# Kernel optimization log

Hardware: AMD Instinct MI355X
Metric: run time of the kernel (lower is better)

The kernel has to match this reference:

```python
import jax, jax.numpy as jnp
import numpy as np

N = 50000        # nodes
E = 800000       # edges
D_IN = 128       # input feature dim
HID = 64         # hidden_dim
HEADS = 4
OUT = 2          # output_dim (fraud / not-fraud)
BN_EPS = 1e-5
NEG_SLOPE = 0.2  # PyG GATv2Conv default


def setup_inputs() -> dict:
    key = jax.random.key(0)
    ks = jax.random.split(key, 16)
    g = lambda k, shape, s=0.05: (jax.random.normal(k, shape, jnp.float32) * s)
    HC = HEADS * HID  # 256
    return {
        "x": jax.random.normal(ks[0], (N, D_IN), jnp.float32),
        "edge_index": jax.random.randint(ks[1], (2, E), 0, N),
        # input projection
        "W_in": g(ks[2], (D_IN, HID)), "b_in": jnp.zeros((HID,), jnp.float32),
        # GATv2 layer 0: HID -> HID, 4 heads (concat -> 256)
        "Wl0": g(ks[3], (HID, HC)), "Wr0": g(ks[4], (HID, HC)),
        "att0": g(ks[5], (HEADS, HID)), "bias0": jnp.zeros((HC,), jnp.float32),
        # GATv2 layer 1: 256 -> HID, 4 heads (concat -> 256)
        "Wl1": g(ks[6], (HC, HC)), "Wr1": g(ks[7], (HC, HC)),
        "att1": g(ks[8], (HEADS, HID)), "bias1": jnp.zeros((HC,), jnp.float32),
        # GATv2 layer 2: 256 -> OUT, 1 head
        "Wl2": g(ks[9], (HC, OUT)), "Wr2": g(ks[10], (HC, OUT)),
        "att2": g(ks[11], (1, OUT)), "bias2": jnp.zeros((OUT,), jnp.float32),
        # BatchNorm (eval mode: running stats) for the first num_layers-1 = 2 layers
        "bn_gamma": jnp.ones((2, HC), jnp.float32),
        "bn_beta": jnp.zeros((2, HC), jnp.float32),
        "bn_mean": jnp.zeros((2, HC), jnp.float32),
        "bn_var": jnp.ones((2, HC), jnp.float32),
    }


def _gatv2(h, src, dst, Wl, Wr, att, bias):
    """PyG GATv2Conv (concat=True, negative_slope=0.2). src->dst messages."""
    n = h.shape[0]
    heads, c = att.shape
    xl = (h @ Wl).reshape(n, heads, c)   # source transform
    xr = (h @ Wr).reshape(n, heads, c)   # target transform
    e = jax.nn.leaky_relu(xl[src] + xr[dst], NEG_SLOPE)       # [E, H, C]
    logits = jnp.einsum('ehc,hc->eh', e, att)                 # [E, H]
    # segment softmax over incoming edges of each destination node
    m = jax.ops.segment_max(logits, dst, num_segments=n)      # [N, H]
    ex = jnp.exp(logits - m[dst])
    denom = jax.ops.segment_sum(ex, dst, num_segments=n)
    alpha = ex / denom[dst]                                   # [E, H]
    out = jax.ops.segment_sum(xl[src] * alpha[..., None], dst, num_segments=n)
    return out.reshape(n, heads * c) + bias


def _bn_eval(h, gamma, beta, mean, var):
    return gamma * (h - mean) * jax.lax.rsqrt(var + BN_EPS) + beta


def reference(x, edge_index, W_in, b_in, Wl0, Wr0, att0, bias0,
              Wl1, Wr1, att1, bias1, Wl2, Wr2, att2, bias2,
              bn_gamma, bn_beta, bn_mean, bn_var):
    n = x.shape[0]
    loop = jnp.arange(n)
    src = jnp.concatenate([edge_index[0], loop])  # PyG add_self_loops=True
    dst = jnp.concatenate([edge_index[1], loop])

    h = jax.nn.relu(x @ W_in + b_in)              # dropout is identity in eval

    # layer 0 (no residual: 64 != 256)
    h = _gatv2(h, src, dst, Wl0, Wr0, att0, bias0)
    h = jax.nn.relu(_bn_eval(h, bn_gamma[0], bn_beta[0], bn_mean[0], bn_var[0]))

    # layer 1 (residual: 256 == 256)
    h_prev = h
    h = _gatv2(h, src, dst, Wl1, Wr1, att1, bias1)
    h = jax.nn.relu(_bn_eval(h, bn_gamma[1], bn_beta[1], bn_mean[1], bn_var[1]))
    h = h + h_prev

    # output layer, 1 head
    h = _gatv2(h, src, dst, Wl2, Wr2, att2, bias2)
    return jax.nn.log_softmax(h, axis=1)
```

## Files before the change

### kernel.cpp

```cpp
#include <hip/hip_runtime.h>
#include <hip/hip_bf16.h>
#include <math.h>


using h16     = _Float16;
using half2v  = __attribute__((ext_vector_type(2))) h16;
using half4v  = __attribute__((ext_vector_type(4))) h16;
using half8   = __attribute__((ext_vector_type(8))) h16;
using floatx2 = __attribute__((ext_vector_type(2))) float;
using floatx4 = __attribute__((ext_vector_type(4))) float;

__device__ __forceinline__ float lrelu(float x) { return x > 0.f ? x : 0.2f * x; }

__device__ __forceinline__ half2v shfl_xor_h2(half2v v, int mask) {
    float f = __builtin_bit_cast(float, v);
    f = __shfl_xor(f, mask, 64);
    return __builtin_bit_cast(half2v, f);
}

__global__ void hist_dst(const int* __restrict__ ei, int E, int* __restrict__ deg) {
    int e = blockIdx.x * blockDim.x + threadIdx.x;
    if (e < E) atomicAdd(&deg[ei[E + e]], 1);
}

__global__ __launch_bounds__(256) void scan_blk(const int* __restrict__ deg,
                                                int* __restrict__ rowstart,
                                                int* __restrict__ bsum, int N) {
    int t = blockIdx.x * 256 + threadIdx.x;
    int lane = threadIdx.x & 63, wid = threadIdx.x >> 6;
    int v = (t < N) ? ((deg[t] + 4) & ~3) : 0;
    int x = v;
#pragma unroll
    for (int off = 1; off < 64; off <<= 1) {
        int y = __shfl_up(x, off, 64);
        if (lane >= off) x += y;
    }
    __shared__ int wsum[4];
    if (lane == 63) wsum[wid] = x;
    __syncthreads();
    int add = 0;
#pragma unroll
    for (int w = 0; w < 4; ++w) if (w < wid) add += wsum[w];
    int incl = x + add;
    if (t < N) rowstart[t] = incl - v;
    if (threadIdx.x == 255) bsum[blockIdx.x] = incl;
}

__global__ __launch_bounds__(256) void scan_off(int* __restrict__ bsum, int NB) {
    int t = threadIdx.x;
    int lane = t & 63, wid = t >> 6;
    int v = (t < NB) ? bsum[t] : 0;
    int x = v;
#pragma unroll
    for (int off = 1; off < 64; off <<= 1) {
        int y = __shfl_up(x, off, 64);
        if (lane >= off) x += y;
    }
    __shared__ int wsum[4];
    if (lane == 63) wsum[wid] = x;
    __syncthreads();
    int add = 0;
#pragma unroll
    for (int w = 0; w < 4; ++w) if (w < wid) add += wsum[w];
    if (t < NB) bsum[t] = x + add - v;
}

__global__ void add_off(const int* __restrict__ bsum, const int* __restrict__ deg,
                        int* __restrict__ rowstart, int* __restrict__ cursor,
                        int* __restrict__ csr_src, int N) {
    int t = blockIdx.x * 256 + threadIdx.x;
    if (t >= N) return;
    int r = rowstart[t] + bsum[blockIdx.x];
    rowstart[t] = r;
    cursor[t] = r;
    int dg = deg[t];
    int npad = (dg + 4) & ~3;
    for (int k = dg; k < npad; ++k) csr_src[r + k] = t;
}

__global__ void scatter_src(const int* __restrict__ ei, int E,
                            int* __restrict__ cursor, int* __restrict__ csr_src) {
    int e = blockIdx.x * blockDim.x + threadIdx.x;
    if (e >= E) return;
    int d = ei[E + e];
    int pos = atomicAdd(&cursor[d], 1);
    csr_src[pos] = ei[e];
}

__device__ __forceinline__ void pack_one(const float* __restrict__ W,
                                         h16* __restrict__ Wp,
                                         int t, int K, int NC) {
    int j = t & 7;
    int l = (t >> 3) & 63;
    int rest = t >> 9;
    int NT = NC >> 4;
    int nt = rest % NT;
    int kc = rest / NT;
    int row = kc * 32 + (l >> 4) * 8 + j;
    int col = nt * 16 + (l & 15);
    Wp[t] = (h16)W[(size_t)row * NC + col];
}

__global__ void pack_all(const float* __restrict__ W_in,
                         const float* __restrict__ Wl0, const float* __restrict__ Wr0,
                         const float* __restrict__ Wl1, const float* __restrict__ Wr1,
                         h16* __restrict__ P_in,
                         h16* __restrict__ P_l0, h16* __restrict__ P_r0,
                         h16* __restrict__ P_l1, h16* __restrict__ P_r1,
                         const float4* __restrict__ x, half4v* __restrict__ xh, int n4,
                         int* __restrict__ deg, int N) {
    int t = blockIdx.x * blockDim.x + threadIdx.x;
    if (t < 8192)        pack_one(W_in, P_in, t, 128, 64);
    else if (t < 24576)  pack_one(Wl0, P_l0, t - 8192, 64, 256);
    else if (t < 40960)  pack_one(Wr0, P_r0, t - 24576, 64, 256);
    else if (t < 106496) pack_one(Wl1, P_l1, t - 40960, 256, 256);
    else if (t < 172032) pack_one(Wr1, P_r1, t - 106496, 256, 256);
    else if (t < 172032 + n4) {
        int u = t - 172032;
        float4 v = x[u];
        half4v o = { (h16)v.x, (h16)v.y, (h16)v.z, (h16)v.w };
        xh[u] = o;
    } else {
        int u = t - 172032 - n4;
        if (u < N) deg[u] = 0;
    }
}

template<int KC, int NT, bool RELU, bool DUAL>
__global__ __launch_bounds__(256) void gemm_lds(
        const h16* __restrict__ Xh,
        const h16* __restrict__ Wp0, const h16* __restrict__ Wp1,
        const float* __restrict__ bias,
        h16* __restrict__ out0, h16* __restrict__ out1, int M) {
    constexpr int K = KC * 32;
    constexpr int ldo = NT * 16;
    constexpr int CHUNK8 = NT * 64;
    constexpr int PER_THR = CHUNK8 / 256;
    __shared__ half8 wbuf[2][CHUNK8];

    const h16* Wp = (DUAL && blockIdx.y) ? Wp1 : Wp0;
    h16* outp = (DUAL && blockIdx.y) ? out1 : out0;
    const half8* WG = (const half8*)Wp;

    const int tid = threadIdx.x;
    const int wid = tid >> 6, lane = tid & 63;
    const int quad = lane >> 4, li = lane & 15;
    const int r0 = blockIdx.x * 64 + wid * 16;
    int arow = r0 + li; if (arow >= M) arow = M - 1;
    const half8* A8 = (const half8*)Xh + (size_t)arow * (K / 8) + quad;

    floatx4 acc[NT];
#pragma unroll
    for (int t = 0; t < NT; ++t) acc[t] = (floatx4){0.f, 0.f, 0.f, 0.f};

    half8 st[PER_THR];
#pragma unroll
    for (int i = 0; i < PER_THR; ++i) st[i] = WG[i * 256 + tid];
#pragma unroll
    for (int i = 0; i < PER_THR; ++i) wbuf[0][i * 256 + tid] = st[i];
    __syncthreads();

#pragma unroll
    for (int kc = 0; kc < KC; ++kc) {
        int cur = kc & 1;
        if (kc + 1 < KC) {
#pragma unroll
            for (int i = 0; i < PER_THR; ++i)
                st[i] = WG[(size_t)(kc + 1) * CHUNK8 + i * 256 + tid];
        }
        half8 a = A8[kc * 4];
#pragma unroll
        for (int nt = 0; nt < NT; ++nt) {
            half8 b = wbuf[cur][nt * 64 + lane];
            acc[nt] = __builtin_amdgcn_mfma_f32_16x16x32_f16(a, b, acc[nt], 0, 0, 0);
        }
        if (kc + 1 < KC) {
#pragma unroll
            for (int i = 0; i < PER_THR; ++i) wbuf[cur ^ 1][i * 256 + tid] = st[i];
        }
        __syncthreads();
    }

#pragma unroll
    for (int nt = 0; nt < NT; ++nt) {
#pragma unroll
        for (int reg = 0; reg < 4; ++reg) {
            int rr = r0 + quad * 4 + reg;
            if (rr >= M) continue;
            float v = acc[nt][reg];
            if (RELU) v = fmaxf(v + bias[nt * 16 + li], 0.f);
            outp[(size_t)rr * ldo + nt * 16 + li] = (h16)v;
        }
    }
}

__global__ void attn4_bn(int N, const h16* __restrict__ XL,
                         const h16* __restrict__ XR,
                         const float* __restrict__ att,
                         const int* __restrict__ rowstart, const int* __restrict__ deg,
                         const int* __restrict__ csr_src,
                         const float* __restrict__ gamma, const float* __restrict__ beta,
                         const float* __restrict__ mean, const float* __restrict__ var,
                         const float* __restrict__ bias, const h16* __restrict__ resid,
                         h16* __restrict__ outb) {
    int wv = blockIdx.x * (blockDim.x >> 6) + (threadIdx.x >> 6);
    int d0 = wv * 2;
    if (d0 >= N) return;
    int lane = threadIdx.x & 63;
    int sl   = lane & 31;
    int dh   = d0 + (lane >> 5);
    bool dvalid = dh < N;
    int dr = dvalid ? dh : d0;

    int start = rowstart[dr];
    int dg    = deg[dr];
    int nreal = dg + 1;
    int npad  = (dg + 4) & ~3;
    int npmax = max(npad, __shfl_xor(npad, 32, 64));

    union H8 { uint4 u; half2v h[4]; };
    H8 bv, wt;
    bv.u = *(const uint4*)(XR + (size_t)dr * 256 + sl * 8);
    {
        const float* ar = att + (sl >> 3) * 64 + (sl & 7) * 8;
        float4 wa = *(const float4*)ar;
        float4 wb = *(const float4*)(ar + 4);
        wt.h[0] = half2v{(h16)wa.x, (h16)wa.y};
        wt.h[1] = half2v{(h16)wa.z, (h16)wa.w};
        wt.h[2] = half2v{(h16)wb.x, (h16)wb.y};
        wt.h[3] = half2v{(h16)wb.z, (h16)wb.w};
    }
    const h16 k02 = (h16)0.2f;
    const uint4* XLv = (const uint4*)XL;

    auto ep = [&](const H8& x) -> h16 {
        half2v q = half2v{(h16)0, (h16)0};
#pragma unroll
        for (int j = 0; j < 4; ++j) {
            half2v e  = x.h[j] + bv.h[j];
            half2v lr = __builtin_elementwise_max(e, e * k02);
            q += lr * wt.h[j];
        }
        return q.x + q.y;
    };

    float l = 0.f;
    half2v acc[4] = {half2v{(h16)0,(h16)0}, half2v{(h16)0,(h16)0},
                     half2v{(h16)0,(h16)0}, half2v{(h16)0,(h16)0}};

    int4 iv = *(const int4*)(csr_src + start);
    for (int i = 0; i < npmax; i += 4) {
        int4 cur = iv;
        if (i + 4 < npmax) {
            int nxt = min(i + 4, npad - 4);
            iv = *(const int4*)(csr_src + start + nxt);
        }
        H8 x0, x1, x2, x3;
        x0.u = XLv[(size_t)(unsigned)cur.x * 32 + sl];
        x1.u = XLv[(size_t)(unsigned)cur.y * 32 + sl];
        x2.u = XLv[(size_t)(unsigned)cur.z * 32 + sl];
        x3.u = XLv[(size_t)(unsigned)cur.w * 32 + sl];
        half2v p01 = { ep(x0), ep(x1) };
        half2v p23 = { ep(x2), ep(x3) };
#pragma unroll
        for (int s = 1; s < 8; s <<= 1) {
            p01 += shfl_xor_h2(p01, s);
            p23 += shfl_xor_h2(p23, s);
        }
        int rem = nreal - i;
        float e0 = (rem > 0) ? __expf((float)p01.x) : 0.f;
        float e1 = (rem > 1) ? __expf((float)p01.y) : 0.f;
        float e2 = (rem > 2) ? __expf((float)p23.x) : 0.f;
        float e3 = (rem > 3) ? __expf((float)p23.y) : 0.f;
        l += (e0 + e1) + (e2 + e3);
        h16 h0 = (h16)e0, h1 = (h16)e1, h2 = (h16)e2, h3 = (h16)e3;
        half2v eb0 = {h0,h0}, eb1 = {h1,h1}, eb2 = {h2,h2}, eb3 = {h3,h3};
#pragma unroll
        for (int j = 0; j < 4; ++j) {
            acc[j] += eb0 * x0.h[j];
            acc[j] += eb1 * x1.h[j];
            acc[j] += eb2 * x2.h[j];
            acc[j] += eb3 * x3.h[j];
        }
    }

    float inv = 1.f / l;
    float oc[8];
#pragma unroll
    for (int j = 0; j < 4; ++j) { oc[2*j] = (float)acc[j].x; oc[2*j+1] = (float)acc[j].y; }
    const float4* g4  = (const float4*)gamma;
    const float4* be4 = (const float4*)beta;
    const float4* mu4 = (const float4*)mean;
    const float4* va4 = (const float4*)var;
    const float4* bi4 = (const float4*)bias;
    float o[8];
#pragma unroll
    for (int q = 0; q < 2; ++q) {
        float4 g  = g4[sl*2+q],  bb = be4[sl*2+q], mu = mu4[sl*2+q];
        float4 va = va4[sl*2+q], bi = bi4[sl*2+q];
        float s0 = g.x * rsqrtf(va.x + 1e-5f);
        float s1 = g.y * rsqrtf(va.y + 1e-5f);
        float s2 = g.z * rsqrtf(va.z + 1e-5f);
        float s3 = g.w * rsqrtf(va.w + 1e-5f);
        o[q*4+0] = fmaxf(oc[q*4+0]*inv*s0 + (bi.x-mu.x)*s0 + bb.x, 0.f);
        o[q*4+1] = fmaxf(oc[q*4+1]*inv*s1 + (bi.y-mu.y)*s1 + bb.y, 0.f);
        o[q*4+2] = fmaxf(oc[q*4+2]*inv*s2 + (bi.z-mu.z)*s2 + bb.z, 0.f);
        o[q*4+3] = fmaxf(oc[q*4+3]*inv*s3 + (bi.w-mu.w)*s3 + bb.w, 0.f);
    }
    if (resid) {
        H8 rv; rv.u = *(const uint4*)(resid + (size_t)dr * 256 + sl * 8);
#pragma unroll
        for (int j = 0; j < 4; ++j) {
            o[2*j]   += (float)rv.h[j].x;
            o[2*j+1] += (float)rv.h[j].y;
        }
    }
    if (dvalid) {
        H8 ov;
#pragma unroll
        for (int j = 0; j < 4; ++j) ov.h[j] = half2v{(h16)o[2*j], (h16)o[2*j+1]};
        *(uint4*)(outb + (size_t)dh * 256 + sl * 8) = ov.u;
    }
}

__global__ void gemm2_wave(const h16* __restrict__ X, const float* __restrict__ Wl,
                           const float* __restrict__ Wr, float* __restrict__ xl2,
                           float* __restrict__ xr2, int N) {
    int t = blockIdx.x * blockDim.x + threadIdx.x;
    int n = t >> 4;
    int sl = t & 15;
    if (n >= N) return;
    const half4v* Xr = (const half4v*)(X + (size_t)n * 256);
    const float4* Wl4 = (const float4*)Wl;
    const float4* Wr4 = (const float4*)Wr;
    float l0 = 0.f, l1 = 0.f, r0 = 0.f, r1 = 0.f;
#pragma unroll
    for (int j = 0; j < 4; ++j) {
        int idx = sl + j * 16;
        half4v xh = Xr[idx];
        float4 xv = { (float)xh.x, (float)xh.y, (float)xh.z, (float)xh.w };
        float4 wa = Wl4[idx * 2];
        float4 wb = Wl4[idx * 2 + 1];
        l0 += xv.x * wa.x + xv.y * wa.z + xv.z * wb.x + xv.w * wb.z;
        l1 += xv.x * wa.y + xv.y * wa.w + xv.z * wb.y + xv.w * wb.w;
        wa = Wr4[idx * 2]; wb = Wr4[idx * 2 + 1];
        r0 += xv.x * wa.x + xv.y * wa.z + xv.z * wb.x + xv.w * wb.z;
        r1 += xv.x * wa.y + xv.y * wa.w + xv.z * wb.y + xv.w * wb.w;
    }
#pragma unroll
    for (int off = 1; off < 16; off <<= 1) {
        l0 += __shfl_xor(l0, off, 64);
        l1 += __shfl_xor(l1, off, 64);
        r0 += __shfl_xor(r0, off, 64);
        r1 += __shfl_xor(r1, off, 64);
    }
    if (sl == 0) {
        xl2[n * 2] = l0; xl2[n * 2 + 1] = l1;
        xr2[n * 2] = r0; xr2[n * 2 + 1] = r1;
    }
}

__global__ void attn1_16(int N, const float* __restrict__ xl2, const float* __restrict__ xr2,
                         const float* __restrict__ att, const float* __restrict__ bias,
                         const int* __restrict__ rowstart, const int* __restrict__ deg,
                         const int* __restrict__ csr_src, float* __restrict__ out) {
    int t = blockIdx.x * blockDim.x + threadIdx.x;
    int d = t >> 4, sl = t & 15;
    if (d >= N) return;
    float a0 = att[0], a1 = att[1];
    float2 xr = ((const float2*)xr2)[d];
    float b0 = xr.x, b1 = xr.y;
    int st = rowstart[d];
    int nreal = deg[d] + 1;
    int npad  = (deg[d] + 4) & ~3;
    float l = 0.f, ac0 = 0.f, ac1 = 0.f;
    for (int i = sl; i < npad; i += 16) {
        int s = csr_src[st + i];
        float2 xv = ((const float2*)xl2)[s];
        float q = lrelu(xv.x + b0) * a0 + lrelu(xv.y + b1) * a1;
        float e = (i < nreal) ? __expf(q) : 0.f;
        l += e; ac0 += e * xv.x; ac1 += e * xv.y;
    }
#pragma unroll
    for (int off = 1; off < 16; off <<= 1) {
        l   += __shfl_xor(l, off, 64);
        ac0 += __shfl_xor(ac0, off, 64);
        ac1 += __shfl_xor(ac1, off, 64);
    }
    if (sl == 0) {
        float inv = 1.f / l;
        float v0 = ac0 * inv + bias[0];
        float v1 = ac1 * inv + bias[1];
        float mx = fmaxf(v0, v1);
        float lse = mx + logf(__expf(v0 - mx) + __expf(v1 - mx));
        out[d * 2] = v0 - lse;
        out[d * 2 + 1] = v1 - lse;
    }
}

extern "C" void kernel_launch(void* const* d_in, const int* in_sizes, int n_in,
                              void* d_out, int out_size, void* d_ws, size_t ws_size,
                              hipStream_t stream) {
    const float* x        = (const float*)d_in[0];
    const int*   ei       = (const int*)  d_in[1];
    const float* W_in     = (const float*)d_in[2];
    const float* b_in     = (const float*)d_in[3];
    const float* Wl0      = (const float*)d_in[4];
    const float* Wr0      = (const float*)d_in[5];
    const float* att0     = (const float*)d_in[6];
    const float* bias0    = (const float*)d_in[7];
    const float* Wl1      = (const float*)d_in[8];
    const float* Wr1      = (const float*)d_in[9];
    const float* att1     = (const float*)d_in[10];
    const float* bias1    = (const float*)d_in[11];
    const float* Wl2      = (const float*)d_in[12];
    const float* Wr2      = (const float*)d_in[13];
    const float* att2     = (const float*)d_in[14];
    const float* bias2    = (const float*)d_in[15];
    const float* bn_gamma = (const float*)d_in[16];
    const float* bn_beta  = (const float*)d_in[17];
    const float* bn_mean  = (const float*)d_in[18];
    const float* bn_var   = (const float*)d_in[19];

    const int N  = in_sizes[0] / 128;
    const int E  = in_sizes[1] / 2;
    const int NB = (N + 255) / 256;

    float* ws = (float*)d_ws;
    size_t off = 0;
    float* XL2  = ws + off; off += (size_t)N * 2;
    float* XR2  = ws + off; off += (size_t)N * 2;
    h16* Ah   = (h16*)(ws + off); off += (size_t)N * 128;
    h16* Bh   = (h16*)(ws + off); off += (size_t)N * 128;
    h16* Ch   = (h16*)(ws + off); off += (size_t)N * 128;
    h16* Dh   = (h16*)(ws + off); off += (size_t)N * 128;
    h16* H0h  = (h16*)(ws + off); off += (size_t)N * 32;
    h16* xh   = (h16*)(ws + off); off += (size_t)N * 64;
    h16* Wp_in = (h16*)(ws + off); off += 4096;
    h16* Wp_l0 = (h16*)(ws + off); off += 8192;
    h16* Wp_r0 = (h16*)(ws + off); off += 8192;
    h16* Wp_l1 = (h16*)(ws + off); off += 32768;
    h16* Wp_r1 = (h16*)(ws + off); off += 32768;
    int* ip = (int*)(ws + off);
    int* deg      = ip;              ip += N;
    int* rowstart = ip;              ip += N;
    int* cursor   = ip;              ip += N;
    int* bsum     = ip;              ip += NB;
    int* csr_src  = ip;              ip += E + 4 * N + 64;

    const int PACK_T = 172032 + N * 32 + N;
    pack_all<<<(PACK_T + 255) / 256, 256, 0, stream>>>(
        W_in, Wl0, Wr0, Wl1, Wr1, Wp_in, Wp_l0, Wp_r0, Wp_l1, Wp_r1,
        (const float4*)x, (half4v*)xh, N * 32, deg, N);

    hist_dst<<<(E + 255) / 256, 256, 0, stream>>>(ei, E, deg);
    scan_blk<<<NB, 256, 0, stream>>>(deg, rowstart, bsum, N);
    scan_off<<<1, 256, 0, stream>>>(bsum, NB);
    add_off<<<NB, 256, 0, stream>>>(bsum, deg, rowstart, cursor, csr_src, N);
    scatter_src<<<(E + 255) / 256, 256, 0, stream>>>(ei, E, cursor, csr_src);

    const int GBM = (N + 63) / 64;

    gemm_lds<4, 4, true, false><<<GBM, 256, 0, stream>>>(
        xh, Wp_in, nullptr, b_in, H0h, nullptr, N);

    gemm_lds<2, 16, false, true><<<dim3(GBM, 2), 256, 0, stream>>>(
        H0h, Wp_l0, Wp_r0, nullptr, Ah, Bh, N);
    attn4_bn<<<(N + 7) / 8, 256, 0, stream>>>(N, Ah, Bh, att0, rowstart, deg, csr_src,
                                              bn_gamma, bn_beta, bn_mean, bn_var,
                                              bias0, nullptr, Ch);

    gemm_lds<8, 16, false, true><<<dim3(GBM, 2), 256, 0, stream>>>(
        Ch, Wp_l1, Wp_r1, nullptr, Ah, Bh, N);
    attn4_bn<<<(N + 7) / 8, 256, 0, stream>>>(N, Ah, Bh, att1, rowstart, deg, csr_src,
                                              bn_gamma + 256, bn_beta + 256, bn_mean + 256,
                                              bn_var + 256, bias1, Ch, Dh);

    gemm2_wave<<<(N * 16 + 255) / 256, 256, 0, stream>>>(Dh, Wl2, Wr2, XL2, XR2, N);
    attn1_16<<<(N * 16 + 255) / 256, 256, 0, stream>>>(N, XL2, XR2, att2, bias2,
                                                       rowstart, deg, csr_src, (float*)d_out);
}
```

Baseline: 405.4 us.

## Degree-bin node permutation, 4 nodes per wave, fuse hist and scatter into other kernels

Nodes are bucketed by padded in-degree into 32 bins, and the resulting permutation drives attn4_bn so each wave handles 4 similar-degree destinations with 16 lanes per node, instead of 2 arbitrary nodes with 32 lanes each. The degree histogram is folded into pack_all and the edge scatter into a combined kernel with the input GEMM, with a memset replacing the in-kernel deg clearing. The aim is to cut load imbalance across a wave and reduce launch count. In exchange, each lane does more per-lane work and uses more registers, and the permuted output writes are scattered.

Result: slower. 982.6 us (+142.4%).

```diff
diff --git a/kernel.cpp b/kernel.cpp
--- a/kernel.cpp
+++ b/kernel.cpp
@@ -18,17 +18,17 @@
     return __builtin_bit_cast(half2v, f);
 }
 
-__global__ void hist_dst(const int* __restrict__ ei, int E, int* __restrict__ deg) {
-    int e = blockIdx.x * blockDim.x + threadIdx.x;
-    if (e < E) atomicAdd(&deg[ei[E + e]], 1);
-}
-
 __global__ __launch_bounds__(256) void scan_blk(const int* __restrict__ deg,
                                                 int* __restrict__ rowstart,
-                                                int* __restrict__ bsum, int N) {
+                                                int* __restrict__ bsum,
+                                                int* __restrict__ bins, int N) {
     int t = blockIdx.x * 256 + threadIdx.x;
     int lane = threadIdx.x & 63, wid = threadIdx.x >> 6;
-    int v = (t < N) ? ((deg[t] + 4) & ~3) : 0;
+    int v = 0;
+    if (t < N) {
+        v = (deg[t] + 4) & ~3;
+        atomicAdd(&bins[min(v >> 2, 31)], 1);
+    }
     int x = v;
 #pragma unroll
     for (int off = 1; off < 64; off <<= 1) {
@@ -46,7 +46,9 @@
     if (threadIdx.x == 255) bsum[blockIdx.x] = incl;
 }
 
-__global__ __launch_bounds__(256) void scan_off(int* __restrict__ bsum, int NB) {
+__global__ __launch_bounds__(256) void scan_off(int* __restrict__ bsum, int NB,
+                                                const int* __restrict__ bins,
+                                                int* __restrict__ bincur) {
     int t = threadIdx.x;
     int lane = t & 63, wid = t >> 6;
     int v = (t < NB) ? bsum[t] : 0;
@@ -63,11 +65,22 @@
 #pragma unroll
     for (int w = 0; w < 4; ++w) if (w < wid) add += wsum[w];
     if (t < NB) bsum[t] = x + add - v;
+    if (t < 32) {
+        int b = bins[t];
+        int xb = b;
+#pragma unroll
+        for (int off2 = 1; off2 < 32; off2 <<= 1) {
+            int y = __shfl_up(xb, off2, 64);
+            if (t >= off2) xb += y;
+        }
+        bincur[t] = xb - b;
+    }
 }
 
 __global__ void add_off(const int* __restrict__ bsum, const int* __restrict__ deg,
                         int* __restrict__ rowstart, int* __restrict__ cursor,
-                        int* __restrict__ csr_src, int N) {
+                        int* __restrict__ csr_src,
+                        int* __restrict__ bincur, int* __restrict__ perm, int N) {
     int t = blockIdx.x * 256 + threadIdx.x;
     if (t >= N) return;
     int r = rowstart[t] + bsum[blockIdx.x];
@@ -76,15 +89,8 @@
     int dg = deg[t];
     int npad = (dg + 4) & ~3;
     for (int k = dg; k < npad; ++k) csr_src[r + k] = t;
-}
-
-__global__ void scatter_src(const int* __restrict__ ei, int E,
-                            int* __restrict__ cursor, int* __restrict__ csr_src) {
-    int e = blockIdx.x * blockDim.x + threadIdx.x;
-    if (e >= E) return;
-    int d = ei[E + e];
-    int pos = atomicAdd(&cursor[d], 1);
-    csr_src[pos] = ei[e];
+    int pos = atomicAdd(&bincur[min(npad >> 2, 31)], 1);
+    perm[pos] = t;
 }
 
 __device__ __forceinline__ void pack_one(const float* __restrict__ W,
@@ -108,7 +114,7 @@
                          h16* __restrict__ P_l0, h16* __restrict__ P_r0,
                          h16* __restrict__ P_l1, h16* __restrict__ P_r1,
                          const float4* __restrict__ x, half4v* __restrict__ xh, int n4,
-                         int* __restrict__ deg, int N) {
+                         const int* __restrict__ ei, int E, int* __restrict__ deg) {
     int t = blockIdx.x * blockDim.x + threadIdx.x;
     if (t < 8192)        pack_one(W_in, P_in, t, 128, 64);
     else if (t < 24576)  pack_one(Wl0, P_l0, t - 8192, 64, 256);
@@ -122,7 +128,71 @@
         xh[u] = o;
     } else {
         int u = t - 172032 - n4;
-        if (u < N) deg[u] = 0;
+        if (u < E) atomicAdd(&deg[ei[E + u]], 1);
+    }
+}
+
+template<int KC, int NT, bool RELU>
+__device__ __forceinline__ void gemm_body(const h16* __restrict__ Xh,
+                                          const h16* __restrict__ Wp,
+                                          const float* __restrict__ bias,
+                                          h16* __restrict__ outp, int M, int bx) {
+    constexpr int K = KC * 32;
+    constexpr int ldo = NT * 16;
+    constexpr int CHUNK8 = NT * 64;
+    constexpr int PER_THR = CHUNK8 / 256;
+    __shared__ half8 wbuf[2][CHUNK8];
+
+    const half8* WG = (const half8*)Wp;
+    const int tid = threadIdx.x;
+    const int wid = tid >> 6, lane = tid & 63;
+    const int quad = lane >> 4, li = lane & 15;
+    const int r0 = bx * 64 + wid * 16;
+    int arow = r0 + li; if (arow >= M) arow = M - 1;
+    const half8* A8 = (const half8*)Xh + (size_t)arow * (K / 8) + quad;
+
+    floatx4 acc[NT];
+#pragma unroll
+    for (int t = 0; t < NT; ++t) acc[t] = (floatx4){0.f, 0.f, 0.f, 0.f};
+
+    half8 st[PER_THR];
+#pragma unroll
+    for (int i = 0; i < PER_THR; ++i) st[i] = WG[i * 256 + tid];
+#pragma unroll
+    for (int i = 0; i < PER_THR; ++i) wbuf[0][i * 256 + tid] = st[i];
+    __syncthreads();
+
+#pragma unroll
+    for (int kc = 0; kc < KC; ++kc) {
+        int cur = kc & 1;
+        if (kc + 1 < KC) {
+#pragma unroll
+            for (int i = 0; i < PER_THR; ++i)
+                st[i] = WG[(size_t)(kc + 1) * CHUNK8 + i * 256 + tid];
+        }
+        half8 a = A8[kc * 4];
+#pragma unroll
+        for (int nt = 0; nt < NT; ++nt) {
+            half8 b = wbuf[cur][nt * 64 + lane];
+            acc[nt] = __builtin_amdgcn_mfma_f32_16x16x32_f16(a, b, acc[nt], 0, 0, 0);
+        }
+        if (kc + 1 < KC) {
+#pragma unroll
+            for (int i = 0; i < PER_THR; ++i) wbuf[cur ^ 1][i * 256 + tid] = st[i];
+        }
+        __syncthreads();
+    }
+
+#pragma unroll
+    for (int nt = 0; nt < NT; ++nt) {
+#pragma unroll
+        for (int reg = 0; reg < 4; ++reg) {
+            int rr = r0 + quad * 4 + reg;
+            if (rr >= M) continue;
+            float v = acc[nt][reg];
+            if (RELU) v = fmaxf(v + bias[nt * 16 + li], 0.f);
+            outp[(size_t)rr * ldo + nt * 16 + li] = (h16)v;
+        }
     }
 }
 
@@ -132,71 +202,32 @@
         const h16* __restrict__ Wp0, const h16* __restrict__ Wp1,
         const float* __restrict__ bias,
         h16* __restrict__ out0, h16* __restrict__ out1, int M) {
-    constexpr int K = KC * 32;
-    constexpr int ldo = NT * 16;
-    constexpr int CHUNK8 = NT * 64;
-    constexpr int PER_THR = CHUNK8 / 256;
-    __shared__ half8 wbuf[2][CHUNK8];
-
     const h16* Wp = (DUAL && blockIdx.y) ? Wp1 : Wp0;
     h16* outp = (DUAL && blockIdx.y) ? out1 : out0;
-    const half8* WG = (const half8*)Wp;
-
-    const int tid = threadIdx.x;
-    const int wid = tid >> 6, lane = tid & 63;
-    const int quad = lane >> 4, li = lane & 15;
-    const int r0 = blockIdx.x * 64 + wid * 16;
-    int arow = r0 + li; if (arow >= M) arow = M - 1;
-    const half8* A8 = (const half8*)Xh + (size_t)arow * (K / 8) + quad;
-
-    floatx4 acc[NT];
-#pragma unroll
-    for (int t = 0; t < NT; ++t) acc[t] = (floatx4){0.f, 0.f, 0.f, 0.f};
-
-    half8 st[PER_THR];
-#pragma unroll
-    for (int i = 0; i < PER_THR; ++i) st[i] = WG[i * 256 + tid];
-#pragma unroll
-    for (int i = 0; i < PER_THR; ++i) wbuf[0][i * 256 + tid] = st[i];
-    __syncthreads();
-
-#pragma unroll
-    for (int kc = 0; kc < KC; ++kc) {
-        int cur = kc & 1;
-        if (kc + 1 < KC) {
-#pragma unroll
-            for (int i = 0; i < PER_THR; ++i)
-                st[i] = WG[(size_t)(kc + 1) * CHUNK8 + i * 256 + tid];
-        }
-        half8 a = A8[kc * 4];
-#pragma unroll
-        for (int nt = 0; nt < NT; ++nt) {
-            half8 b = wbuf[cur][nt * 64 + lane];
-            acc[nt] = __builtin_amdgcn_mfma_f32_16x16x32_f16(a, b, acc[nt], 0, 0, 0);
-        }
-        if (kc + 1 < KC) {
-#pragma unroll
-            for (int i = 0; i < PER_THR; ++i) wbuf[cur ^ 1][i * 256 + tid] = st[i];
-        }
-        __syncthreads();
-    }
-
-#pragma unroll
-    for (int nt = 0; nt < NT; ++nt) {
-#pragma unroll
-        for (int reg = 0; reg < 4; ++reg) {
-            int rr = r0 + quad * 4 + reg;
-            if (rr >= M) continue;
-            float v = acc[nt][reg];
-            if (RELU) v = fmaxf(v + bias[nt * 16 + li], 0.f);
-            outp[(size_t)rr * ldo + nt * 16 + li] = (h16)v;
-        }
+    gemm_body<KC, NT, RELU>(Xh, Wp, bias, outp, M, blockIdx.x);
+}
+
+__global__ __launch_bounds__(256) void scatter_gemm0(
+        const int* __restrict__ ei, int E,
+        int* __restrict__ cursor, int* __restrict__ csr_src, int GS,
+        const h16* __restrict__ xh, const h16* __restrict__ Wp_in,
+        const float* __restrict__ b_in, h16* __restrict__ H0h, int M) {
+    if ((int)blockIdx.x < GS) {
+        int e = blockIdx.x * 256 + threadIdx.x;
+        if (e < E) {
+            int d = ei[E + e];
+            int pos = atomicAdd(&cursor[d], 1);
+            csr_src[pos] = ei[e];
+        }
+    } else {
+        gemm_body<4, 4, true>(xh, Wp_in, b_in, H0h, M, blockIdx.x - GS);
     }
 }
 
 __global__ void attn4_bn(int N, const h16* __restrict__ XL,
                          const h16* __restrict__ XR,
                          const float* __restrict__ att,
+                         const int* __restrict__ perm,
                          const int* __restrict__ rowstart, const int* __restrict__ deg,
                          const int* __restrict__ csr_src,
                          const float* __restrict__ gamma, const float* __restrict__ beta,
@@ -204,39 +235,40 @@
                          const float* __restrict__ bias, const h16* __restrict__ resid,
                          h16* __restrict__ outb) {
     int wv = blockIdx.x * (blockDim.x >> 6) + (threadIdx.x >> 6);
-    int d0 = wv * 2;
-    if (d0 >= N) return;
+    if (wv * 4 >= N) return;
     int lane = threadIdx.x & 63;
-    int sl   = lane & 31;
-    int dh   = d0 + (lane >> 5);
-    bool dvalid = dh < N;
-    int dr = dvalid ? dh : d0;
-
-    int start = rowstart[dr];
-    int dg    = deg[dr];
+    int sl   = lane & 15;
+    int idx  = wv * 4 + (lane >> 4);
+    bool dvalid = idx < N;
+    int dh = perm[dvalid ? idx : (N - 1)];
+
+    int start = rowstart[dh];
+    int dg    = deg[dh];
     int nreal = dg + 1;
     int npad  = (dg + 4) & ~3;
-    int npmax = max(npad, __shfl_xor(npad, 32, 64));
-
-    union H8 { uint4 u; half2v h[4]; };
-    H8 bv, wt;
-    bv.u = *(const uint4*)(XR + (size_t)dr * 256 + sl * 8);
+    int m1    = max(npad, __shfl_xor(npad, 16, 64));
+    int npmax = max(m1, __shfl_xor(m1, 32, 64));
+
+    union H16 { uint4 u[2]; half2v h[8]; };
+    H16 bv, wt;
+    bv.u[0] = *(const uint4*)(XR + (size_t)dh * 256 + sl * 16);
+    bv.u[1] = *(const uint4*)(XR + (size_t)dh * 256 + sl * 16 + 8);
     {
-        const float* ar = att + (sl >> 3) * 64 + (sl & 7) * 8;
-        float4 wa = *(const float4*)ar;
-        float4 wb = *(const float4*)(ar + 4);
-        wt.h[0] = half2v{(h16)wa.x, (h16)wa.y};
-        wt.h[1] = half2v{(h16)wa.z, (h16)wa.w};
-        wt.h[2] = half2v{(h16)wb.x, (h16)wb.y};
-        wt.h[3] = half2v{(h16)wb.z, (h16)wb.w};
+        const float* ar = att + sl * 16;
+#pragma unroll
+        for (int q = 0; q < 4; ++q) {
+            float4 w = *(const float4*)(ar + q * 4);
+            wt.h[2*q]   = half2v{(h16)w.x, (h16)w.y};
+            wt.h[2*q+1] = half2v{(h16)w.z, (h16)w.w};
+        }
     }
     const h16 k02 = (h16)0.2f;
     const uint4* XLv = (const uint4*)XL;
 
-    auto ep = [&](const H8& x) -> h16 {
-        half2v q = half2v{(h16)0, (h16)0};
-#pragma unroll
-        for (int j = 0; j < 4; ++j) {
+    auto ep = [&](const H16& x) -> h16 {
+        half2v q{(h16)0, (h16)0};
+#pragma unroll
+        for (int j = 0; j < 8; ++j) {
             half2v e  = x.h[j] + bv.h[j];
             half2v lr = __builtin_elementwise_max(e, e * k02);
             q += lr * wt.h[j];
@@ -245,8 +277,9 @@
     };
 
     float l = 0.f;
-    half2v acc[4] = {half2v{(h16)0,(h16)0}, half2v{(h16)0,(h16)0},
-                     half2v{(h16)0,(h16)0}, half2v{(h16)0,(h16)0}};
+    half2v acc[8];
+#pragma unroll
+    for (int j = 0; j < 8; ++j) acc[j] = half2v{(h16)0, (h16)0};
 
     int4 iv = *(const int4*)(csr_src + start);
     for (int i = 0; i < npmax; i += 4) {
@@ -255,15 +288,19 @@
             int nxt = min(i + 4, npad - 4);
             iv = *(const int4*)(csr_src + start + nxt);
         }
-        H8 x0, x1, x2, x3;
-        x0.u = XLv[(size_t)(unsigned)cur.x * 32 + sl];
-        x1.u = XLv[(size_t)(unsigned)cur.y * 32 + sl];
-        x2.u = XLv[(size_t)(unsigned)cur.z * 32 + sl];
-        x3.u = XLv[(size_t)(unsigned)cur.w * 32 + sl];
+        H16 x0, x1, x2, x3;
+        size_t a0 = (size_t)(unsigned)cur.x * 32 + sl * 2;
+        size_t a1 = (size_t)(unsigned)cur.y * 32 + sl * 2;
+        size_t a2 = (size_t)(unsigned)cur.z * 32 + sl * 2;
+        size_t a3 = (size_t)(unsigned)cur.w * 32 + sl * 2;
+        x0.u[0] = XLv[a0]; x0.u[1] = XLv[a0 + 1];
+        x1.u[0] = XLv[a1]; x1.u[1] = XLv[a1 + 1];
+        x2.u[0] = XLv[a2]; x2.u[1] = XLv[a2 + 1];
+        x3.u[0] = XLv[a3]; x3.u[1] = XLv[a3 + 1];
         half2v p01 = { ep(x0), ep(x1) };
         half2v p23 = { ep(x2), ep(x3) };
 #pragma unroll
-        for (int s = 1; s < 8; s <<= 1) {
+        for (int s = 1; s < 4; s <<= 1) {
             p01 += shfl_xor_h2(p01, s);
             p23 += shfl_xor_h2(p23, s);
         }
@@ -274,9 +311,9 @@
         float e3 = (rem > 3) ? __expf((float)p23.y) : 0.f;
         l += (e0 + e1) + (e2 + e3);
         h16 h0 = (h16)e0, h1 = (h16)e1, h2 = (h16)e2, h3 = (h16)e3;
-        half2v eb0 = {h0,h0}, eb1 = {h1,h1}, eb2 = {h2,h2}, eb3 = {h3,h3};
-#pragma unroll
-        for (int j = 0; j < 4; ++j) {
+        half2v eb0{h0,h0}, eb1{h1,h1}, eb2{h2,h2}, eb3{h3,h3};
+#pragma unroll
+        for (int j = 0; j < 8; ++j) {
             acc[j] += eb0 * x0.h[j];
             acc[j] += eb1 * x1.h[j];
             acc[j] += eb2 * x2.h[j];
@@ -285,19 +322,20 @@
     }
 
     float inv = 1.f / l;
-    float oc[8];
-#pragma unroll
-    for (int j = 0; j < 4; ++j) { oc[2*j] = (float)acc[j].x; oc[2*j+1] = (float)acc[j].y; }
+    float oc[16];
+#pragma unroll
+    for (int j = 0; j < 8; ++j) { oc[2*j] = (float)acc[j].x; oc[2*j+1] = (float)acc[j].y; }
     const float4* g4  = (const float4*)gamma;
     const float4* be4 = (const float4*)beta;
     const float4* mu4 = (const float4*)mean;
     const float4* va4 = (const float4*)var;
     const float4* bi4 = (const float4*)bias;
-    float o[8];
-#pragma unroll
-    for (int q = 0; q < 2; ++q) {
-        float4 g  = g4[sl*2+q],  bb = be4[sl*2+q], mu = mu4[sl*2+q];
-        float4 va = va4[sl*2+q], bi = bi4[sl*2+q];
+    float o[16];
+#pragma unroll
+    for (int q = 0; q < 4; ++q) {
+        int ci = sl * 4 + q;
+        float4 g  = g4[ci], bb = be4[ci], mu = mu4[ci];
+        float4 va = va4[ci], bi = bi4[ci];
         float s0 = g.x * rsqrtf(va.x + 1e-5f);
         float s1 = g.y * rsqrtf(va.y + 1e-5f);
         float s2 = g.z * rsqrtf(va.z + 1e-5f);
@@ -308,18 +346,21 @@
         o[q*4+3] = fmaxf(oc[q*4+3]*inv*s3 + (bi.w-mu.w)*s3 + bb.w, 0.f);
     }
     if (resid) {
-        H8 rv; rv.u = *(const uint4*)(resid + (size_t)dr * 256 + sl * 8);
-#pragma unroll
-        for (int j = 0; j < 4; ++j) {
+        H16 rv;
+        rv.u[0] = *(const uint4*)(resid + (size_t)dh * 256 + sl * 16);
+        rv.u[1] = *(const uint4*)(resid + (size_t)dh * 256 + sl * 16 + 8);
+#pragma unroll
+        for (int j = 0; j < 8; ++j) {
             o[2*j]   += (float)rv.h[j].x;
             o[2*j+1] += (float)rv.h[j].y;
         }
     }
     if (dvalid) {
-        H8 ov;
-#pragma unroll
-        for (int j = 0; j < 4; ++j) ov.h[j] = half2v{(h16)o[2*j], (h16)o[2*j+1]};
-        *(uint4*)(outb + (size_t)dh * 256 + sl * 8) = ov.u;
+        H16 ov;
+#pragma unroll
+        for (int j = 0; j < 8; ++j) ov.h[j] = half2v{(h16)o[2*j], (h16)o[2*j+1]};
+        *(uint4*)(outb + (size_t)dh * 256 + sl * 16)     = ov.u[0];
+        *(uint4*)(outb + (size_t)dh * 256 + sl * 16 + 8) = ov.u[1];
     }
 }
 
@@ -443,38 +484,45 @@
     h16* Wp_r1 = (h16*)(ws + off); off += 32768;
     int* ip = (int*)(ws + off);
     int* deg      = ip;              ip += N;
+    int* bins     = ip;              ip += 32;
+    int* bincur   = ip;              ip += 32;
     int* rowstart = ip;              ip += N;
     int* cursor   = ip;              ip += N;
     int* bsum     = ip;              ip += NB;
+    int* perm     = ip;              ip += N;
     int* csr_src  = ip;              ip += E + 4 * N + 64;
 
-    const int PACK_T = 172032 + N * 32 + N;
+    hipMemsetAsync(deg, 0, (size_t)(N + 32) * sizeof(int), stream);
+
+    const int PACK_T = 172032 + N * 32 + E;
     pack_all<<<(PACK_T + 255) / 256, 256, 0, stream>>>(
         W_in, Wl0, Wr0, Wl1, Wr1, Wp_in, Wp_l0, Wp_r0, Wp_l1, Wp_r1,
-        (const float4*)x, (half4v*)xh, N * 32, deg, N);
-
-    hist_dst<<<(E + 255) / 256, 256, 0, stream>>>(ei, E, deg);
-    scan_blk<<<NB, 256, 0, stream>>>(deg, rowstart, bsum, N);
-    scan_off<<<1, 256, 0, stream>>>(bsum, NB);
-    add_off<<<NB, 256, 0, stream>>>(bsum, deg, rowstart, cursor, csr_src, N);
-    scatter_src<<<(E + 255) / 256, 256, 0, stream>>>(ei, E, cursor, csr_src);
+        (const float4*)x, (half4v*)xh, N * 32, ei, E, deg);
+
+    scan_blk<<<NB, 256, 0, stream>>>(deg, rowstart, bsum, bins, N);
+    scan_off<<<1, 256, 0, stream>>>(bsum, NB, bins, bincur);
+    add_off<<<NB, 256, 0, stream>>>(bsum, deg, rowstart, cursor, csr_src,
+                                    bincur, perm, N);
 
     const int GBM = (N + 63) / 64;
-
-    gemm_lds<4, 4, true, false><<<GBM, 256, 0, stream>>>(
-        xh, Wp_in, nullptr, b_in, H0h, nullptr, N);
+    const int GS  = (E + 255) / 256;
+
+    scatter_gemm0<<<GS + GBM, 256, 0, stream>>>(ei, E, cursor, csr_src, GS,
+                                                xh, Wp_in, b_in, H0h, N);
 
     gemm_lds<2, 16, false, true><<<dim3(GBM, 2), 256, 0, stream>>>(
         H0h, Wp_l0, Wp_r0, nullptr, Ah, Bh, N);
-    attn4_bn<<<(N + 7) / 8, 256, 0, stream>>>(N, Ah, Bh, att0, rowstart, deg, csr_src,
-                                              bn_gamma, bn_beta, bn_mean, bn_var,
-                                              bias0, nullptr, Ch);
+    attn4_bn<<<(N + 15) / 16, 256, 0, stream>>>(N, Ah, Bh, att0, perm,
+                                                rowstart, deg, csr_src,
+                                                bn_gamma, bn_beta, bn_mean, bn_var,
+                                                bias0, nullptr, Ch);
 
     gemm_lds<8, 16, false, true><<<dim3(GBM, 2), 256, 0, stream>>>(
         Ch, Wp_l1, Wp_r1, nullptr, Ah, Bh, N);
-    attn4_bn<<<(N + 7) / 8, 256, 0, stream>>>(N, Ah, Bh, att1, rowstart, deg, csr_src,
-                                              bn_gamma + 256, bn_beta + 256, bn_mean + 256,
-                                              bn_var + 256, bias1, Ch, Dh);
+    attn4_bn<<<(N + 15) / 16, 256, 0, stream>>>(N, Ah, Bh, att1, perm,
+                                                rowstart, deg, csr_src,
+                                                bn_gamma + 256, bn_beta + 256, bn_mean + 256,
+                                                bn_var + 256, bias1, Ch, Dh);
 
     gemm2_wave<<<(N * 16 + 255) / 256, 256, 0, stream>>>(Dh, Wl2, Wr2, XL2, XR2, N);
     attn1_16<<<(N * 16 + 255) / 256, 256, 0, stream>>>(N, XL2, XR2, att2, bias2,
```

## Fuse degree histogram into pack kernel and scatter into input GEMM

Applied to the files above, without the earlier changes.

Degree zeroing moves to a memset so the destination-degree histogram can run inside the weight/feature packing kernel. The CSR scatter kernel and the input projection GEMM are merged into one launch, with block ranges split between edge scattering (4 edges per thread, loads batched for memory-level parallelism) and GEMM tiles. This cuts two kernel launches and lets independent work overlap. The cost is mixed block roles, and the gemm body is refactored into a shared device function.

Result: faster. 397.1 us (-2.1%).

```diff
diff --git a/kernel.cpp b/kernel.cpp
--- a/kernel.cpp
+++ b/kernel.cpp
@@ -16,11 +16,6 @@
     float f = __builtin_bit_cast(float, v);
     f = __shfl_xor(f, mask, 64);
     return __builtin_bit_cast(half2v, f);
-}
-
-__global__ void hist_dst(const int* __restrict__ ei, int E, int* __restrict__ deg) {
-    int e = blockIdx.x * blockDim.x + threadIdx.x;
-    if (e < E) atomicAdd(&deg[ei[E + e]], 1);
 }
 
 __global__ __launch_bounds__(256) void scan_blk(const int* __restrict__ deg,
@@ -76,15 +71,6 @@
     int dg = deg[t];
     int npad = (dg + 4) & ~3;
     for (int k = dg; k < npad; ++k) csr_src[r + k] = t;
-}
-
-__global__ void scatter_src(const int* __restrict__ ei, int E,
-                            int* __restrict__ cursor, int* __restrict__ csr_src) {
-    int e = blockIdx.x * blockDim.x + threadIdx.x;
-    if (e >= E) return;
-    int d = ei[E + e];
-    int pos = atomicAdd(&cursor[d], 1);
-    csr_src[pos] = ei[e];
 }
 
 __device__ __forceinline__ void pack_one(const float* __restrict__ W,
@@ -108,7 +94,7 @@
                          h16* __restrict__ P_l0, h16* __restrict__ P_r0,
                          h16* __restrict__ P_l1, h16* __restrict__ P_r1,
                          const float4* __restrict__ x, half4v* __restrict__ xh, int n4,
-                         int* __restrict__ deg, int N) {
+                         const int* __restrict__ ei, int E, int* __restrict__ deg) {
     int t = blockIdx.x * blockDim.x + threadIdx.x;
     if (t < 8192)        pack_one(W_in, P_in, t, 128, 64);
     else if (t < 24576)  pack_one(Wl0, P_l0, t - 8192, 64, 256);
@@ -122,7 +108,71 @@
         xh[u] = o;
     } else {
         int u = t - 172032 - n4;
-        if (u < N) deg[u] = 0;
+        if (u < E) atomicAdd(&deg[ei[E + u]], 1);
+    }
+}
+
+template<int KC, int NT, bool RELU>
+__device__ __forceinline__ void gemm_body(const h16* __restrict__ Xh,
+                                          const h16* __restrict__ Wp,
+                                          const float* __restrict__ bias,
+                                          h16* __restrict__ outp, int M, int bx) {
+    constexpr int K = KC * 32;
+    constexpr int ldo = NT * 16;
+    constexpr int CHUNK8 = NT * 64;
+    constexpr int PER_THR = CHUNK8 / 256;
+    __shared__ half8 wbuf[2][CHUNK8];
+
+    const half8* WG = (const half8*)Wp;
+    const int tid = threadIdx.x;
+    const int wid = tid >> 6, lane = tid & 63;
+    const int quad = lane >> 4, li = lane & 15;
+    const int r0 = bx * 64 + wid * 16;
+    int arow = r0 + li; if (arow >= M) arow = M - 1;
+    const half8* A8 = (const half8*)Xh + (size_t)arow * (K / 8) + quad;
+
+    floatx4 acc[NT];
+#pragma unroll
+    for (int t = 0; t < NT; ++t) acc[t] = (floatx4){0.f, 0.f, 0.f, 0.f};
+
+    half8 st[PER_THR];
+#pragma unroll
+    for (int i = 0; i < PER_THR; ++i) st[i] = WG[i * 256 + tid];
+#pragma unroll
+    for (int i = 0; i < PER_THR; ++i) wbuf[0][i * 256 + tid] = st[i];
+    __syncthreads();
+
+#pragma unroll
+    for (int kc = 0; kc < KC; ++kc) {
+        int cur = kc & 1;
+        if (kc + 1 < KC) {
+#pragma unroll
+            for (int i = 0; i < PER_THR; ++i)
+                st[i] = WG[(size_t)(kc + 1) * CHUNK8 + i * 256 + tid];
+        }
+        half8 a = A8[kc * 4];
+#pragma unroll
+        for (int nt = 0; nt < NT; ++nt) {
+            half8 b = wbuf[cur][nt * 64 + lane];
+            acc[nt] = __builtin_amdgcn_mfma_f32_16x16x32_f16(a, b, acc[nt], 0, 0, 0);
+        }
+        if (kc + 1 < KC) {
+#pragma unroll
+            for (int i = 0; i < PER_THR; ++i) wbuf[cur ^ 1][i * 256 + tid] = st[i];
+        }
+        __syncthreads();
+    }
+
+#pragma unroll
+    for (int nt = 0; nt < NT; ++nt) {
+#pragma unroll
+        for (int reg = 0; reg < 4; ++reg) {
+            int rr = r0 + quad * 4 + reg;
+            if (rr >= M) continue;
+            float v = acc[nt][reg];
+            if (RELU) v = fmaxf(v + bias[nt * 16 + li], 0.f);
+            outp[(size_t)rr * ldo + nt * 16 + li] = (h16)v;
+        }
     }
 }
 
@@ -132,65 +182,37 @@
         const h16* __restrict__ Wp0, const h16* __restrict__ Wp1,
         const float* __restrict__ bias,
         h16* __restrict__ out0, h16* __restrict__ out1, int M) {
-    constexpr int K = KC * 32;
-    constexpr int ldo = NT * 16;
-    constexpr int CHUNK8 = NT * 64;
-    constexpr int PER_THR = CHUNK8 / 256;
-    __shared__ half8 wbuf[2][CHUNK8];
-
     const h16* Wp = (DUAL && blockIdx.y) ? Wp1 : Wp0;
     h16* outp = (DUAL && blockIdx.y) ? out1 : out0;
-    const half8* WG = (const half8*)Wp;
-
-    const int tid = threadIdx.x;
-    const int wid = tid >> 6, lane = tid & 63;
-    const int quad = lane >> 4, li = lane & 15;
-    const int r0 = blockIdx.x * 64 + wid * 16;
-    int arow = r0 + li; if (arow >= M) arow = M - 1;
-    const half8* A8 = (const half8*)Xh + (size_t)arow * (K / 8) + quad;
-
-    floatx4 acc[NT];
-#pragma unroll
-    for (int t = 0; t < NT; ++t) acc[t] = (floatx4){0.f, 0.f, 0.f, 0.f};
-
-    half8 st[PER_THR];
-#pragma unroll
-    for (int i = 0; i < PER_THR; ++i) st[i] = WG[i * 256 + tid];
-#pragma unroll
-    for (int i = 0; i < PER_THR; ++i) wbuf[0][i * 256 + tid] = st[i];
-    __syncthreads();
-
-#pragma unroll
-    for (int kc = 0; kc < KC; ++kc) {
-        int cur = kc & 1;
-        if (kc + 1 < KC) {
-#pragma unroll
-            for (int i = 0; i < PER_THR; ++i)
-                st[i] = WG[(size_t)(kc + 1) * CHUNK8 + i * 256 + tid];
-        }
-        half8 a = A8[kc * 4];
-#pragma unroll
-        for (int nt = 0; nt < NT; ++nt) {
-            half8 b = wbuf[cur][nt * 64 + lane];
-            acc[nt] = __builtin_amdgcn_mfma_f32_16x16x32_f16(a, b, acc[nt], 0, 0, 0);
-        }
-        if (kc + 1 < KC) {
-#pragma unroll
-            for (int i = 0; i < PER_THR; ++i) wbuf[cur ^ 1][i * 256 + tid] = st[i];
-        }
-        __syncthreads();
-    }
-
-#pragma unroll
-    for (int nt = 0; nt < NT; ++nt) {
-#pragma unroll
-        for (int reg = 0; reg < 4; ++reg) {
-            int rr = r0 + quad * 4 + reg;
-            if (rr >= M) continue;
-            float v = acc[nt][reg];
-            if (RELU) v = fmaxf(v + bias[nt * 16 + li], 0.f);
-            outp[(size_t)rr * ldo + nt * 16 + li] = (h16)v;
-        }
+    gemm_body<KC, NT, RELU>(Xh, Wp, bias, outp, M, blockIdx.x);
+}
+
+__global__ __launch_bounds__(256) void scatter_gemm0(
+        const int* __restrict__ ei, int E,
+        int* __restrict__ cursor, int* __restrict__ csr_src, int GS,
+        const h16* __restrict__ xh, const h16* __restrict__ Wp_in,
+        const float* __restrict__ b_in, h16* __restrict__ H0h, int M) {
+    if ((int)blockIdx.x < GS) {
+        int base = blockIdx.x * 1024 + threadIdx.x;
+        int e0 = base, e1 = base + 256, e2 = base + 512, e3 = base + 768;
+        int d0 = (e0 < E) ? ei[E + e0] : 0;
+        int d1 = (e1 < E) ? ei[E + e1] : 0;
+        int d2 = (e2 < E) ? ei[E + e2] : 0;
+        int d3 = (e3 < E) ? ei[E + e3] : 0;
+        int p0 = (e0 < E) ? atomicAdd(&cursor[d0], 1) : 0;
+        int p1 = (e1 < E) ? atomicAdd(&cursor[d1], 1) : 0;
+        int p2 = (e2 < E) ? atomicAdd(&cursor[d2], 1) : 0;
+        int p3 = (e3 < E) ? atomicAdd(&cursor[d3], 1) : 0;
+        int s0 = (e0 < E) ? ei[e0] : 0;
+        int s1 = (e1 < E) ? ei[e1] : 0;
+        int s2 = (e2 < E) ? ei[e2] : 0;
+        int s3 = (e3 < E) ? ei[e3] : 0;
+        if (e0 < E) csr_src[p0] = s0;
+        if (e1 < E) csr_src[p1] = s1;
+        if (e2 < E) csr_src[p2] = s2;
+        if (e3 < E) csr_src[p3] = s3;
+    } else {
+        gemm_body<4, 4, true>(xh, Wp_in, b_in, H0h, M, blockIdx.x - GS);
     }
 }
 
@@ -234,7 +256,7 @@
     const uint4* XLv = (const uint4*)XL;
 
     auto ep = [&](const H8& x) -> h16 {
-        half2v q = half2v{(h16)0, (h16)0};
+        half2v q{(h16)0, (h16)0};
 #pragma unroll
         for (int j = 0; j < 4; ++j) {
             half2v e  = x.h[j] + bv.h[j];
@@ -274,7 +296,7 @@
         float e3 = (rem > 3) ? __expf((float)p23.y) : 0.f;
         l += (e0 + e1) + (e2 + e3);
         h16 h0 = (h16)e0, h1 = (h16)e1, h2 = (h16)e2, h3 = (h16)e3;
-        half2v eb0 = {h0,h0}, eb1 = {h1,h1}, eb2 = {h2,h2}, eb3 = {h3,h3};
+        half2v eb0{h0,h0}, eb1{h1,h1}, eb2{h2,h2}, eb3{h3,h3};
 #pragma unroll
         for (int j = 0; j < 4; ++j) {
             acc[j] += eb0 * x0.h[j];
@@ -448,31 +470,34 @@
     int* bsum     = ip;              ip += NB;
     int* csr_src  = ip;              ip += E + 4 * N + 64;
 
-    const int PACK_T = 172032 + N * 32 + N;
+    hipMemsetAsync(deg, 0, (size_t)N * sizeof(int), stream);
+
+    const int PACK_T = 172032 + N * 32 + E;
     pack_all<<<(PACK_T + 255) / 256, 256, 0, stream>>>(
         W_in, Wl0, Wr0, Wl1, Wr1, Wp_in, Wp_l0, Wp_r0, Wp_l1, Wp_r1,
-        (const float4*)x, (half4v*)xh, N * 32, deg, N);
-
-    hist_dst<<<(E + 255) / 256, 256, 0, stream>>>(ei, E, deg);
+        (const float4*)x, (half4v*)xh, N * 32, ei, E, deg);
+
     scan_blk<<<NB, 256, 0, stream>>>(deg, rowstart, bsum, N);
     scan_off<<<1, 256, 0, stream>>>(bsum, NB);
     add_off<<<NB, 256, 0, stream>>>(bsum, deg, rowstart, cursor, csr_src, N);
-    scatter_src<<<(E + 255) / 256, 256, 0, stream>>>(ei, E, cursor, csr_src);
 
     const int GBM = (N + 63) / 64;
-
-    gemm_lds<4, 4, true, false><<<GBM, 256, 0, stream>>>(
-        xh, Wp_in, nullptr, b_in, H0h, nullptr, N);
+    const int GS  = (E + 1023) / 1024;
+
+    scatter_gemm0<<<GS + GBM, 256, 0, stream>>>(ei, E, cursor, csr_src, GS,
+                                                xh, Wp_in, b_in, H0h, N);
 
     gemm_lds<2, 16, false, true><<<dim3(GBM, 2), 256, 0, stream>>>(
         H0h, Wp_l0, Wp_r0, nullptr, Ah, Bh, N);
-    attn4_bn<<<(N + 7) / 8, 256, 0, stream>>>(N, Ah, Bh, att0, rowstart, deg, csr_src,
+    attn4_bn<<<(N + 7) / 8, 256, 0, stream>>>(N, Ah, Bh, att0,
+                                              rowstart, deg, csr_src,
                                               bn_gamma, bn_beta, bn_mean, bn_var,
                                               bias0, nullptr, Ch);
 
     gemm_lds<8, 16, false, true><<<dim3(GBM, 2), 256, 0, stream>>>(
         Ch, Wp_l1, Wp_r1, nullptr, Ah, Bh, N);
-    attn4_bn<<<(N + 7) / 8, 256, 0, stream>>>(N, Ah, Bh, att1, rowstart, deg, csr_src,
+    attn4_bn<<<(N + 7) / 8, 256, 0, stream>>>(N, Ah, Bh, att1,
+                                              rowstart, deg, csr_src,
                                               bn_gamma + 256, bn_beta + 256, bn_mean + 256,
                                               bn_var + 256, bias1, Ch, Dh);
 
```
